# Kernel optimization log

Hardware: AMD Instinct MI355X
Metric: run time of the kernel (lower is better)

## Reference

```python
import jax, jax.numpy as jnp
import numpy as np

ATTR_LEN = [2, 4, 4, 2, 6]
CUM = np.concatenate(([0], np.cumsum(ATTR_LEN)))  # [0,2,6,10,12,18]
B, S, D, V = 4096, 200, 64, 100000


def setup_inputs() -> dict:
    key = jax.random.key(0)
    ks = jax.random.split(key, 10)
    x = jax.random.randint(ks[0], (B, S), 0, V)
    # one-hot labels per attribute, concatenated -> [B, 18]
    y_parts = []
    for i, al in enumerate(ATTR_LEN):
        lab = jax.random.randint(jax.random.fold_in(ks[1], i), (B,), 0, al)
        y_parts.append(jax.nn.one_hot(lab, al, dtype=jnp.float32))
    y = jnp.concatenate(y_parts, axis=1)
    emb_table = jax.random.normal(ks[2], (V, D), jnp.float32) * 0.02
    emb_table = emb_table.at[0].set(0.0)  # padding_idx=0
    att_w = jax.random.normal(ks[3], (5, D), jnp.float32) * 0.1
    att_b = jax.random.normal(ks[4], (5,), jnp.float32) * 0.1
    W0 = jax.random.normal(ks[5], (ATTR_LEN[0], D), jnp.float32) * 0.1
    W1 = jax.random.normal(ks[6], (ATTR_LEN[1], D), jnp.float32) * 0.1
    W2 = jax.random.normal(ks[7], (ATTR_LEN[2], D), jnp.float32) * 0.1
    W3 = jax.random.normal(ks[8], (ATTR_LEN[3], D), jnp.float32) * 0.1
    W4 = jax.random.normal(ks[9], (ATTR_LEN[4], D), jnp.float32) * 0.1
    return {"x": x, "y": y, "emb_table": emb_table, "att_w": att_w,
            "att_b": att_b, "W0": W0, "W1": W1, "W2": W2, "W3": W3, "W4": W4}


def reference(x, y, emb_table, att_w, att_b, W0, W1, W2, W3, W4):
    embed = emb_table[x]  # [B, S, D] gather (padding row is zero)
    # 5 per-attribute additive tanh-attention heads, batched over k.
    # Softmax over seq axis is independent per head, so stacking is exact.
    att_u = jnp.tanh(jnp.einsum('bsd,kd->bsk', embed, att_w) + att_b)  # [B,S,5]
    score = jax.nn.softmax(att_u, axis=1)                              # [B,S,5]
    user_rep = jnp.einsum('bsd,bsk->bkd', embed, score)                # [B,5,D]
    Ws = [W0, W1, W2, W3, W4]
    # per-task bias-free linear heads, concatenated -> [B, 18]
    W_user = jnp.concatenate([user_rep[:, i] @ Ws[i].T for i in range(5)], axis=1)
    logits = []
    loss = jnp.float32(0.0)
    for i in range(5):
        Wc = W_user[:, CUM[i]:CUM[i + 1]]
        yc = y[:, CUM[i]:CUM[i + 1]]
        # partial_training=False -> ob = ones -> all rows kept;
        # obj = exp(sum(W*y)) / sum_j exp(W_j)  ==  softmax picked at label
        logp = jax.nn.log_softmax(Wc, axis=1)
        loss = loss + (-jnp.sum(logp * yc) / Wc.shape[0])
        logits.append(jax.nn.softmax(Wc, axis=1))
    logit = jnp.concatenate(logits, axis=1)  # [B, 18]
    return logit, loss
```

## Files before the change

### kernel.cpp

```cpp
#include <hip/hip_runtime.h>
#include <math.h>
#include <stdint.h>

#define Bsz 4096
#define Ssz 200
#define Dsz 64
#define NK  5
#define NT  512
#define RST 72
#define TST 232
#define UNIH 14848

typedef _Float16 half_t;
typedef _Float16 h2    __attribute__((ext_vector_type(2)));
typedef _Float16 f16x8 __attribute__((ext_vector_type(8)));
typedef float    f32x4 __attribute__((ext_vector_type(4)));

__device__ inline h2 pk(float a, float b) {
    return __builtin_bit_cast(h2, __builtin_amdgcn_cvt_pkrtz(a, b));
}

__device__ inline float fast_tanh(float x) {
    float e = __expf(-2.0f * fabsf(x));
    float r = (1.0f - e) / (1.0f + e);
    return copysignf(r, x);
}

__device__ inline void phase_bar() {
    asm volatile("s_waitcnt lgkmcnt(0)" ::: "memory");
    __builtin_amdgcn_s_barrier();
    __builtin_amdgcn_sched_barrier(0);
}

__global__ void zero_loss_kernel(float* loss) {
    if (threadIdx.x == 0) *loss = 0.0f;
}

__global__ __launch_bounds__(256) void cvt_kernel(const float* __restrict__ src,
                                                  half_t* __restrict__ dst) {
    const size_t i = ((size_t)blockIdx.x * 256 + threadIdx.x) * 8;
    if (i < (size_t)100000 * 64) {
        float4 v0 = *(const float4*)(src + i);
        float4 v1 = *(const float4*)(src + i + 4);
        union { half_t h[8]; uint4 u; } o;
        o.h[0] = (half_t)v0.x; o.h[1] = (half_t)v0.y;
        o.h[2] = (half_t)v0.z; o.h[3] = (half_t)v0.w;
        o.h[4] = (half_t)v1.x; o.h[5] = (half_t)v1.y;
        o.h[6] = (half_t)v1.z; o.h[7] = (half_t)v1.w;
        *(uint4*)(dst + i) = o.u;
    }
}

__device__ inline void head_phase(int b, const float* wu, const float* __restrict__ y,
                                  float* __restrict__ out_logit, float& lossacc, int l) {
    if (l < NK) {
        const int LEN[5] = {2, 4, 4, 2, 6};
        const int C0[5]  = {0, 2, 6, 10, 12};
        const int g = l, c0 = C0[g], len = LEN[g];
        float* op = out_logit + (size_t)b * 18;
        const float* yp = y + (size_t)b * 18;
        float mx = -1e30f;
        for (int j = 0; j < len; ++j) mx = fmaxf(mx, wu[c0 + j]);
        float sum = 0.f;
        for (int j = 0; j < len; ++j) sum += __expf(wu[c0 + j] - mx);
        float inv = 1.0f / sum;
        float lse = mx + __logf(sum);
        for (int j = 0; j < len; ++j) {
            op[c0 + j] = __expf(wu[c0 + j] - mx) * inv;
            lossacc += (lse - wu[c0 + j]) * yp[c0 + j];
        }
    }
}

__global__ __launch_bounds__(NT, 8) void tan2_kernel(
    const int* __restrict__ x, const float* __restrict__ y,
    const half_t* __restrict__ tab16,
    const float* __restrict__ att_w, const float* __restrict__ att_b,
    const float* __restrict__ W0, const float* __restrict__ W1,
    const float* __restrict__ W2, const float* __restrict__ W3,
    const float* __restrict__ W4,
    float* __restrict__ out_logit, float* __restrict__ loss_out)
{
    __shared__ alignas(16) half_t uni[UNIH];
    __shared__ alignas(16) float  ovl[1000];
    __shared__ alignas(16) half_t ascore[NK * 240];
    __shared__ alignas(16) half_t awh[NK * RST];
    __shared__ float wu[18];

    half_t* embR = uni;
    half_t* embT = uni;
    float*  att_raw = ovl;

    const int blk = blockIdx.x;
    const int b0  = 2 * blk, b1 = 2 * blk + 1;
    const int tid = threadIdx.x;
    const int w   = tid >> 6;
    const int l   = tid & 63;
    const int col = l & 15;
    const int kg  = l >> 4;

    float lossacc = 0.f;

    {
        uint4 z = {0u, 0u, 0u, 0u};
        if (tid < 200)
            *(uint4*)((char*)uni + tid * 144 + 128) = z;
        else if (tid < 256)
            *(uint4*)((char*)uni + 28800 + (tid - 200) * 16) = z;
    }
    if (tid >= 256 && tid < 256 + NK * 32) {
        const int t = tid - 256, row = t >> 5, cp = t & 31;
        h2 v = {(half_t)att_w[row * 64 + 2 * cp],
                (half_t)att_w[row * 64 + 2 * cp + 1]};
        *(h2*)(awh + row * RST + 2 * cp) = v;
    }
    uint4 ga[4], gb[4];
#pragma unroll
    for (int p = 0; p < 4; ++p) {
        int i = tid + NT * p;
        if (i > 1599) i = 1599;
        const int s = i >> 3, c = i & 7;
        ga[p] = *(const uint4*)(tab16 + (size_t)x[b0 * Ssz + s] * Dsz + c * 8);
    }
#pragma unroll
    for (int p = 0; p < 4; ++p) {
        int i = tid + NT * p;
        if (i > 1599) i = 1599;
        const int s = i >> 3, c = i & 7;
        gb[p] = *(const uint4*)(tab16 + (size_t)x[b1 * Ssz + s] * Dsz + c * 8);
    }
#pragma unroll
    for (int p = 0; p < 4; ++p) {
        const int i = tid + NT * p;
        if (p < 3 || i < 1600) {
            const int s = i >> 3, c = i & 7;
            *(uint4*)(embR + s * RST + c * 8) = ga[p];
        }
    }
    phase_bar();

    h2 te[4][4];
#pragma unroll 1
    for (int bb = 0; bb < 2; ++bb) {
#pragma unroll
        for (int p = 0; p < 4; ++p) {
            int t = tid + NT * p;
            if (t > 1599) t = 1599;
            const int dp = t & 31, sq = t >> 5;
#pragma unroll
            for (int r = 0; r < 4; ++r)
                te[p][r] = *(const h2*)(embR + (4 * sq + r) * RST + 2 * dp);
        }
        {
            const int brow = (col < 5) ? col : 0;
            const f16x8 bw0 = *(const f16x8*)(awh + brow * RST + kg * 8);
            const f16x8 bw1 = *(const f16x8*)(awh + brow * RST + 32 + kg * 8);
            const float bk = att_b[brow];
            for (int t = w; t < 13; t += 8) {
                const int s  = 16 * t + col;
                const int sr = (s < Ssz) ? s : (Ssz - 1);
                const f16x8 a0 = *(const f16x8*)(embR + sr * RST + kg * 8);
                const f16x8 a1 = *(const f16x8*)(embR + sr * RST + 32 + kg * 8);
                f32x4 acc = {0.f, 0.f, 0.f, 0.f};
                acc = __builtin_amdgcn_mfma_f32_16x16x32_f16(a0, bw0, acc, 0, 0, 0);
                acc = __builtin_amdgcn_mfma_f32_16x16x32_f16(a1, bw1, acc, 0, 0, 0);
                if (col < 5) {
#pragma unroll
                    for (int r = 0; r < 4; ++r) {
                        const int srow = 16 * t + 4 * kg + r;
                        if (srow < Ssz)
                            att_raw[col * 200 + srow] = fast_tanh(acc[r] + bk);
                    }
                }
            }
        }
        if (bb == 1 && w == 0) head_phase(b0, wu, y, out_logit, lossacc, l);
        phase_bar();

#pragma unroll
        for (int p = 0; p < 4; ++p) {
            const int t = tid + NT * p;
            if (t < 1600) {
                const int dp = t & 31, sq = t >> 5;
                h2 lo01 = {te[p][0].x, te[p][1].x}, lo23 = {te[p][2].x, te[p][3].x};
                h2 hi01 = {te[p][0].y, te[p][1].y}, hi23 = {te[p][2].y, te[p][3].y};
                uint2 ulo = { __builtin_bit_cast(unsigned, lo01),
                              __builtin_bit_cast(unsigned, lo23) };
                uint2 uhi = { __builtin_bit_cast(unsigned, hi01),
                              __builtin_bit_cast(unsigned, hi23) };
                *(uint2*)(embT + (2 * dp)     * TST + 4 * sq) = ulo;
                *(uint2*)(embT + (2 * dp + 1) * TST + 4 * sq) = uhi;
            }
        }
        if (w < NK) {
            const int k = w;
            float vals[4];
            float mx = -1e30f;
#pragma unroll
            for (int j = 0; j < 4; ++j) {
                const int s = l + 64 * j;
                vals[j] = (s < Ssz) ? att_raw[k * 200 + s] : -1e30f;
                mx = fmaxf(mx, vals[j]);
            }
#pragma unroll
            for (int m = 32; m >= 1; m >>= 1) mx = fmaxf(mx, __shfl_xor(mx, m));
            float sum = 0.f;
#pragma unroll
            for (int j = 0; j < 4; ++j) {
                vals[j] = __expf(vals[j] - mx);
                sum += vals[j];
            }
#pragma unroll
            for (int m = 32; m >= 1; m >>= 1) sum += __shfl_xor(sum, m);
            const float inv = 1.0f / sum;
#pragma unroll
            for (int j = 0; j < 4; ++j) {
                const int s = l + 64 * j;
                if (s < Ssz)      ascore[k * 240 + s] = (half_t)(vals[j] * inv);
                else if (s < 224) ascore[k * 240 + s] = (half_t)0.0f;
            }
        }
        phase_bar();

        {
            const int dtile = w & 3, hh = w >> 2;
            const int arow = (col < 5) ? col : 0;
            const int KK0 = hh ? 4 : 0;
            const int NKK = hh ? 3 : 4;
            f32x4 acc = {0.f, 0.f, 0.f, 0.f};
            for (int q = 0; q < NKK; ++q) {
                const int kk = KK0 + q;
                const f16x8 af = *(const f16x8*)(embT + (dtile * 16 + col) * TST
                                                 + kk * 32 + kg * 8);
                const f16x8 bf = *(const f16x8*)(ascore + arow * 240 + kk * 32 + kg * 8);
                acc = __builtin_amdgcn_mfma_f32_16x16x32_f16(af, bf, acc, 0, 0, 0);
            }
            float* urp = ovl + hh * 320;
            if (col < 5) {
#pragma unroll
                for (int r = 0; r < 4; ++r)
                    urp[col * 64 + dtile * 16 + 4 * kg + r] = acc[r];
            }
        }
        phase_bar();

        if (bb == 0) {
#pragma unroll
            for (int p = 0; p < 4; ++p) {
                const int i = tid + NT * p;
                if (p < 3 || i < 1600) {
                    const int s = i >> 3, c = i & 7;
                    *(uint4*)(embR + s * RST + c * 8) = gb[p];
                }
            }
        }
        for (int j = w; j < 18; j += 8) {
            const float* Wp; int gr, c0;
            if      (j < 2)  { gr = 0; c0 = 0;  Wp = W0; }
            else if (j < 6)  { gr = 1; c0 = 2;  Wp = W1; }
            else if (j < 10) { gr = 2; c0 = 6;  Wp = W2; }
            else if (j < 12) { gr = 3; c0 = 10; Wp = W3; }
            else             { gr = 4; c0 = 12; Wp = W4; }
            float p = (ovl[gr * 64 + l] + ovl[320 + gr * 64 + l])
                      * Wp[(j - c0) * Dsz + l];
#pragma unroll
            for (int m = 32; m >= 1; m >>= 1) p += __shfl_xor(p, m);
            if (l == 0) wu[j] = p;
        }
        phase_bar();
    }

    if (w == 0) {
        head_phase(b1, wu, y, out_logit, lossacc, l);
#pragma unroll
        for (int m = 1; m <= 4; m <<= 1) lossacc += __shfl_xor(lossacc, m);
        if (l == 0) atomicAdd(loss_out, lossacc * (1.0f / Bsz));
    }
}

__global__ __launch_bounds__(NT, 8) void tan1_kernel(
    const int* __restrict__ x, const float* __restrict__ y,
    const float* __restrict__ emb_table,
    const float* __restrict__ att_w, const float* __restrict__ att_b,
    const float* __restrict__ W0, const float* __restrict__ W1,
    const float* __restrict__ W2, const float* __restrict__ W3,
    const float* __restrict__ W4,
    float* __restrict__ out_logit, float* __restrict__ loss_out)
{
    __shared__ alignas(16) half_t uni[UNIH];
    __shared__ alignas(16) float  ovl[1000];
    __shared__ alignas(16) half_t ascore[NK * 240];
    __shared__ alignas(16) half_t awh[NK * RST];
    __shared__ alignas(16) int    xs[Ssz];
    __shared__ float wu[18];

    half_t* embR = uni;
    half_t* embT = uni;
    float*  att_raw = ovl;

    const int b   = blockIdx.x;
    const int tid = threadIdx.x;
    const int w   = tid >> 6;
    const int l   = tid & 63;
    const int col = l & 15;
    const int kg  = l >> 4;

    if (tid < Ssz) xs[tid] = x[b * Ssz + tid];
    {
        uint4 z = {0u, 0u, 0u, 0u};
        if (tid >= 200 && tid < 400)
            *(uint4*)((char*)uni + (tid - 200) * 144 + 128) = z;
        else if (tid >= 400 && tid < 456)
            *(uint4*)((char*)uni + 28800 + (tid - 400) * 16) = z;
    }
    if (tid >= 456 && tid < 456 + 40) {
        const int t = tid - 456, row = t >> 3, cp = t & 7;
        h2 v0 = {(half_t)att_w[row * 64 + 8 * cp + 0], (half_t)att_w[row * 64 + 8 * cp + 1]};
        h2 v1 = {(half_t)att_w[row * 64 + 8 * cp + 2], (half_t)att_w[row * 64 + 8 * cp + 3]};
        h2 v2 = {(half_t)att_w[row * 64 + 8 * cp + 4], (half_t)att_w[row * 64 + 8 * cp + 5]};
        h2 v3 = {(half_t)att_w[row * 64 + 8 * cp + 6], (half_t)att_w[row * 64 + 8 * cp + 7]};
        *(h2*)(awh + row * RST + 8 * cp + 0) = v0;
        *(h2*)(awh + row * RST + 8 * cp + 2) = v1;
        *(h2*)(awh + row * RST + 8 * cp + 4) = v2;
        *(h2*)(awh + row * RST + 8 * cp + 6) = v3;
    }
    __syncthreads();
    {
        float4 v[7];
#pragma unroll
        for (int p = 0; p < 7; ++p) {
            int i = tid + NT * p;
            if (i > Ssz * 16 - 1) i = Ssz * 16 - 1;
            const int s = i >> 4, c = i & 15;
            v[p] = ((const float4*)(emb_table + (size_t)xs[s] * Dsz))[c];
        }
#pragma unroll
        for (int p = 0; p < 7; ++p) {
            const int i = tid + NT * p;
            if (p < 6 || i < Ssz * 16) {
                const int s = i >> 4, c = i & 15;
                h2 lo = pk(v[p].x, v[p].y);
                h2 hi = pk(v[p].z, v[p].w);
                uint2 u = { __builtin_bit_cast(unsigned, lo),
                            __builtin_bit_cast(unsigned, hi) };
                *(uint2*)(embR + s * RST + c * 4) = u;
            }
        }
    }
    __syncthreads();
    h2 te[4][4];
#pragma unroll
    for (int p = 0; p < 4; ++p) {
        int t = tid + NT * p;
        if (t > 1599) t = 1599;
        const int dp = t & 31, sq = t >> 5;
#pragma unroll
        for (int r = 0; r < 4; ++r)
            te[p][r] = *(const h2*)(embR + (4 * sq + r) * RST + 2 * dp);
    }
    {
        const int brow = (col < 5) ? col : 0;
        const f16x8 bw0 = *(const f16x8*)(awh + brow * RST + kg * 8);
        const f16x8 bw1 = *(const f16x8*)(awh + brow * RST + 32 + kg * 8);
        const float bk = att_b[brow];
        for (int t = w; t < 13; t += 8) {
            const int s  = 16 * t + col;
            const int sr = (s < Ssz) ? s : (Ssz - 1);
            const f16x8 a0 = *(const f16x8*)(embR + sr * RST + kg * 8);
            const f16x8 a1 = *(const f16x8*)(embR + sr * RST + 32 + kg * 8);
            f32x4 acc = {0.f, 0.f, 0.f, 0.f};
            acc = __builtin_amdgcn_mfma_f32_16x16x32_f16(a0, bw0, acc, 0, 0, 0);
            acc = __builtin_amdgcn_mfma_f32_16x16x32_f16(a1, bw1, acc, 0, 0, 0);
            if (col < 5) {
#pragma unroll
                for (int r = 0; r < 4; ++r) {
                    const int srow = 16 * t + 4 * kg + r;
                    if (srow < Ssz)
                        att_raw[col * 200 + srow] = fast_tanh(acc[r] + bk);
                }
            }
        }
    }
    __syncthreads();
#pragma unroll
    for (int p = 0; p < 4; ++p) {
        const int t = tid + NT * p;
        if (t < 1600) {
            const int dp = t & 31, sq = t >> 5;
            h2 lo01 = {te[p][0].x, te[p][1].x}, lo23 = {te[p][2].x, te[p][3].x};
            h2 hi01 = {te[p][0].y, te[p][1].y}, hi23 = {te[p][2].y, te[p][3].y};
            uint2 ulo = { __builtin_bit_cast(unsigned, lo01),
                          __builtin_bit_cast(unsigned, lo23) };
            uint2 uhi = { __builtin_bit_cast(unsigned, hi01),
                          __builtin_bit_cast(unsigned, hi23) };
            *(uint2*)(embT + (2 * dp)     * TST + 4 * sq) = ulo;
            *(uint2*)(embT + (2 * dp + 1) * TST + 4 * sq) = uhi;
        }
    }
    if (w < NK) {
        const int k = w;
        float vals[4];
        float mx = -1e30f;
#pragma unroll
        for (int j = 0; j < 4; ++j) {
            const int s = l + 64 * j;
            vals[j] = (s < Ssz) ? att_raw[k * 200 + s] : -1e30f;
            mx = fmaxf(mx, vals[j]);
        }
#pragma unroll
        for (int m = 32; m >= 1; m >>= 1) mx = fmaxf(mx, __shfl_xor(mx, m));
        float sum = 0.f;
#pragma unroll
        for (int j = 0; j < 4; ++j) {
            vals[j] = __expf(vals[j] - mx);
            sum += vals[j];
        }
#pragma unroll
        for (int m = 32; m >= 1; m >>= 1) sum += __shfl_xor(sum, m);
        const float inv = 1.0f / sum;
#pragma unroll
        for (int j = 0; j < 4; ++j) {
            const int s = l + 64 * j;
            if (s < Ssz)      ascore[k * 240 + s] = (half_t)(vals[j] * inv);
            else if (s < 224) ascore[k * 240 + s] = (half_t)0.0f;
        }
    }
    __syncthreads();
    {
        const int dtile = w & 3, hh = w >> 2;
        const int arow = (col < 5) ? col : 0;
        const int KK0 = hh ? 4 : 0;
        const int NKK = hh ? 3 : 4;
        f32x4 acc = {0.f, 0.f, 0.f, 0.f};
        for (int q = 0; q < NKK; ++q) {
            const int kk = KK0 + q;
            const f16x8 af = *(const f16x8*)(embT + (dtile * 16 + col) * TST
                                             + kk * 32 + kg * 8);
            const f16x8 bf = *(const f16x8*)(ascore + arow * 240 + kk * 32 + kg * 8);
            acc = __builtin_amdgcn_mfma_f32_16x16x32_f16(af, bf, acc, 0, 0, 0);
        }
        float* urp = ovl + hh * 320;
        if (col < 5) {
#pragma unroll
            for (int r = 0; r < 4; ++r)
                urp[col * 64 + dtile * 16 + 4 * kg + r] = acc[r];
        }
    }
    __syncthreads();
    for (int j = w; j < 18; j += 8) {
        const float* Wp; int gr, c0;
        if      (j < 2)  { gr = 0; c0 = 0;  Wp = W0; }
        else if (j < 6)  { gr = 1; c0 = 2;  Wp = W1; }
        else if (j < 10) { gr = 2; c0 = 6;  Wp = W2; }
        else if (j < 12) { gr = 3; c0 = 10; Wp = W3; }
        else             { gr = 4; c0 = 12; Wp = W4; }
        float p = (ovl[gr * 64 + l] + ovl[320 + gr * 64 + l]) * Wp[(j - c0) * Dsz + l];
#pragma unroll
        for (int m = 32; m >= 1; m >>= 1) p += __shfl_xor(p, m);
        if (l == 0) wu[j] = p;
    }
    __syncthreads();
    if (w == 0) {
        float lossb = 0.f;
        head_phase(b, wu, y, out_logit, lossb, l);
#pragma unroll
        for (int m = 1; m <= 4; m <<= 1) lossb += __shfl_xor(lossb, m);
        if (l == 0) atomicAdd(loss_out, lossb * (1.0f / Bsz));
    }
}

extern "C" void kernel_launch(void* const* d_in, const int* in_sizes, int n_in,
                              void* d_out, int out_size, void* d_ws, size_t ws_size,
                              hipStream_t stream) {
    const int*   x   = (const int*)d_in[0];
    const float* y   = (const float*)d_in[1];
    const float* emb = (const float*)d_in[2];
    const float* aw  = (const float*)d_in[3];
    const float* ab  = (const float*)d_in[4];
    const float* W0  = (const float*)d_in[5];
    const float* W1  = (const float*)d_in[6];
    const float* W2  = (const float*)d_in[7];
    const float* W3  = (const float*)d_in[8];
    const float* W4  = (const float*)d_in[9];
    float* out  = (float*)d_out;
    float* loss = out + (size_t)Bsz * 18;

    zero_loss_kernel<<<1, 64, 0, stream>>>(loss);

    const size_t need = (size_t)100000 * 64 * sizeof(half_t);
    if (d_ws && ws_size >= need) {
        half_t* tab16 = (half_t*)d_ws;
        cvt_kernel<<<3125, 256, 0, stream>>>(emb, tab16);
        tan2_kernel<<<Bsz / 2, NT, 0, stream>>>(x, y, tab16, aw, ab,
                                                W0, W1, W2, W3, W4, out, loss);
    } else {
        tan1_kernel<<<Bsz, NT, 0, stream>>>(x, y, emb, aw, ab,
                                            W0, W1, W2, W3, W4, out, loss);
    }
}
```

Before: 171.7 us.

## Gather first batch row directly to LDS with XOR-swizzled unpadded layout

Result: faster. 166.9 us (-2.8%).

```diff
diff --git a/kernel.cpp b/kernel.cpp
--- a/kernel.cpp
+++ b/kernel.cpp
@@ -7,7 +7,7 @@
 #define Dsz 64
 #define NK  5
 #define NT  512
-#define RST 72
+#define AWST 72
 #define TST 232
 #define UNIH 14848
 
@@ -72,7 +72,7 @@
     }
 }
 
-__global__ __launch_bounds__(NT, 8) void tan2_kernel(
+__global__ __launch_bounds__(NT, 6) void tan2_kernel(
     const int* __restrict__ x, const float* __restrict__ y,
     const half_t* __restrict__ tab16,
     const float* __restrict__ att_w, const float* __restrict__ att_b,
@@ -84,7 +84,7 @@
     __shared__ alignas(16) half_t uni[UNIH];
     __shared__ alignas(16) float  ovl[1000];
     __shared__ alignas(16) half_t ascore[NK * 240];
-    __shared__ alignas(16) half_t awh[NK * RST];
+    __shared__ alignas(16) half_t awh[NK * AWST];
     __shared__ float wu[18];
 
     half_t* embR = uni;
@@ -101,42 +101,50 @@
 
     float lossacc = 0.f;
 
-    {
+    if (tid < 256) {
         uint4 z = {0u, 0u, 0u, 0u};
-        if (tid < 200)
-            *(uint4*)((char*)uni + tid * 144 + 128) = z;
-        else if (tid < 256)
-            *(uint4*)((char*)uni + 28800 + (tid - 200) * 16) = z;
+        *(uint4*)((char*)uni + 25600 + tid * 16) = z;
     }
     if (tid >= 256 && tid < 256 + NK * 32) {
         const int t = tid - 256, row = t >> 5, cp = t & 31;
         h2 v = {(half_t)att_w[row * 64 + 2 * cp],
                 (half_t)att_w[row * 64 + 2 * cp + 1]};
-        *(h2*)(awh + row * RST + 2 * cp) = v;
-    }
-    uint4 ga[4], gb[4];
+        *(h2*)(awh + row * AWST + 2 * cp) = v;
+    }
+
+    int xr0[4], xr1[4];
 #pragma unroll
     for (int p = 0; p < 4; ++p) {
         int i = tid + NT * p;
         if (i > 1599) i = 1599;
-        const int s = i >> 3, c = i & 7;
-        ga[p] = *(const uint4*)(tab16 + (size_t)x[b0 * Ssz + s] * Dsz + c * 8);
-    }
+        const int s = i >> 3;
+        xr0[p] = x[b0 * Ssz + s];
+        xr1[p] = x[b1 * Ssz + s];
+    }
+
+#pragma unroll
+    for (int p = 0; p < 4; ++p) {
+        if (p < 3 || tid < 64) {
+            const int i = tid + NT * p;
+            const int s = i >> 3, c = i & 7;
+            const half_t* gp = tab16 + (size_t)xr0[p] * Dsz + ((c ^ (s & 7)) << 3);
+            char* lp = (char*)uni + ((size_t)((tid & ~63) + NT * p) << 4);
+            __builtin_amdgcn_global_load_lds(
+                (const __attribute__((address_space(1))) void*)gp,
+                (__attribute__((address_space(3))) void*)lp, 16, 0, 0);
+        }
+    }
+    __builtin_amdgcn_sched_barrier(0);
+    uint4 gb[4];
 #pragma unroll
     for (int p = 0; p < 4; ++p) {
         int i = tid + NT * p;
         if (i > 1599) i = 1599;
-        const int s = i >> 3, c = i & 7;
-        gb[p] = *(const uint4*)(tab16 + (size_t)x[b1 * Ssz + s] * Dsz + c * 8);
-    }
-#pragma unroll
-    for (int p = 0; p < 4; ++p) {
-        const int i = tid + NT * p;
-        if (p < 3 || i < 1600) {
-            const int s = i >> 3, c = i & 7;
-            *(uint4*)(embR + s * RST + c * 8) = ga[p];
-        }
-    }
+        const int c = i & 7;
+        gb[p] = *(const uint4*)(tab16 + (size_t)xr1[p] * Dsz + c * 8);
+    }
+    __builtin_amdgcn_sched_barrier(0);
+    asm volatile("s_waitcnt vmcnt(4)" ::: "memory");
     phase_bar();
 
     h2 te[4][4];
@@ -148,19 +156,24 @@
             if (t > 1599) t = 1599;
             const int dp = t & 31, sq = t >> 5;
 #pragma unroll
-            for (int r = 0; r < 4; ++r)
-                te[p][r] = *(const h2*)(embR + (4 * sq + r) * RST + 2 * dp);
+            for (int r = 0; r < 4; ++r) {
+                const int s4 = 4 * sq + r;
+                te[p][r] = *(const h2*)(embR + s4 * 64
+                                        + (((dp >> 2) ^ (s4 & 7)) << 3)
+                                        + (dp & 3) * 2);
+            }
         }
         {
             const int brow = (col < 5) ? col : 0;
-            const f16x8 bw0 = *(const f16x8*)(awh + brow * RST + kg * 8);
-            const f16x8 bw1 = *(const f16x8*)(awh + brow * RST + 32 + kg * 8);
+            const f16x8 bw0 = *(const f16x8*)(awh + brow * AWST + kg * 8);
+            const f16x8 bw1 = *(const f16x8*)(awh + brow * AWST + 32 + kg * 8);
             const float bk = att_b[brow];
             for (int t = w; t < 13; t += 8) {
                 const int s  = 16 * t + col;
                 const int sr = (s < Ssz) ? s : (Ssz - 1);
-                const f16x8 a0 = *(const f16x8*)(embR + sr * RST + kg * 8);
-                const f16x8 a1 = *(const f16x8*)(embR + sr * RST + 32 + kg * 8);
+                const int c0 = kg ^ (sr & 7);
+                const f16x8 a0 = *(const f16x8*)(embR + sr * 64 + (c0 << 3));
+                const f16x8 a1 = *(const f16x8*)(embR + sr * 64 + ((c0 ^ 4) << 3));
                 f32x4 acc = {0.f, 0.f, 0.f, 0.f};
                 acc = __builtin_amdgcn_mfma_f32_16x16x32_f16(a0, bw0, acc, 0, 0, 0);
                 acc = __builtin_amdgcn_mfma_f32_16x16x32_f16(a1, bw1, acc, 0, 0, 0);
@@ -250,19 +263,19 @@
                 const int i = tid + NT * p;
                 if (p < 3 || i < 1600) {
                     const int s = i >> 3, c = i & 7;
-                    *(uint4*)(embR + s * RST + c * 8) = gb[p];
+                    *(uint4*)(embR + s * 64 + ((c ^ (s & 7)) << 3)) = gb[p];
                 }
             }
         }
         for (int j = w; j < 18; j += 8) {
-            const float* Wp; int gr, c0;
-            if      (j < 2)  { gr = 0; c0 = 0;  Wp = W0; }
-            else if (j < 6)  { gr = 1; c0 = 2;  Wp = W1; }
-            else if (j < 10) { gr = 2; c0 = 6;  Wp = W2; }
-            else if (j < 12) { gr = 3; c0 = 10; Wp = W3; }
-            else             { gr = 4; c0 = 12; Wp = W4; }
+            const float* Wp; int gr, c0w;
+            if      (j < 2)  { gr = 0; c0w = 0;  Wp = W0; }
+            else if (j < 6)  { gr = 1; c0w = 2;  Wp = W1; }
+            else if (j < 10) { gr = 2; c0w = 6;  Wp = W2; }
+            else if (j < 12) { gr = 3; c0w = 10; Wp = W3; }
+            else             { gr = 4; c0w = 12; Wp = W4; }
             float p = (ovl[gr * 64 + l] + ovl[320 + gr * 64 + l])
-                      * Wp[(j - c0) * Dsz + l];
+                      * Wp[(j - c0w) * Dsz + l];
 #pragma unroll
             for (int m = 32; m >= 1; m >>= 1) p += __shfl_xor(p, m);
             if (l == 0) wu[j] = p;
@@ -278,7 +291,7 @@
     }
 }
 
-__global__ __launch_bounds__(NT, 8) void tan1_kernel(
+__global__ __launch_bounds__(NT, 6) void tan1_kernel(
     const int* __restrict__ x, const float* __restrict__ y,
     const float* __restrict__ emb_table,
     const float* __restrict__ att_w, const float* __restrict__ att_b,
@@ -287,6 +300,7 @@
     const float* __restrict__ W4,
     float* __restrict__ out_logit, float* __restrict__ loss_out)
 {
+#define RST 72
     __shared__ alignas(16) half_t uni[UNIH];
     __shared__ alignas(16) float  ovl[1000];
     __shared__ alignas(16) half_t ascore[NK * 240];
@@ -448,13 +462,13 @@
     }
     __syncthreads();
     for (int j = w; j < 18; j += 8) {
-        const float* Wp; int gr, c0;
-        if      (j < 2)  { gr = 0; c0 = 0;  Wp = W0; }
-        else if (j < 6)  { gr = 1; c0 = 2;  Wp = W1; }
-        else if (j < 10) { gr = 2; c0 = 6;  Wp = W2; }
-        else if (j < 12) { gr = 3; c0 = 10; Wp = W3; }
-        else             { gr = 4; c0 = 12; Wp = W4; }
-        float p = (ovl[gr * 64 + l] + ovl[320 + gr * 64 + l]) * Wp[(j - c0) * Dsz + l];
+        const float* Wp; int gr, c0w;
+        if      (j < 2)  { gr = 0; c0w = 0;  Wp = W0; }
+        else if (j < 6)  { gr = 1; c0w = 2;  Wp = W1; }
+        else if (j < 10) { gr = 2; c0w = 6;  Wp = W2; }
+        else if (j < 12) { gr = 3; c0w = 10; Wp = W3; }
+        else             { gr = 4; c0w = 12; Wp = W4; }
+        float p = (ovl[gr * 64 + l] + ovl[320 + gr * 64 + l]) * Wp[(j - c0w) * Dsz + l];
 #pragma unroll
         for (int m = 32; m >= 1; m >>= 1) p += __shfl_xor(p, m);
         if (l == 0) wu[j] = p;
@@ -467,6 +481,7 @@
         for (int m = 1; m <= 4; m <<= 1) lossb += __shfl_xor(lossb, m);
         if (l == 0) atomicAdd(loss_out, lossb * (1.0f / Bsz));
     }
+#undef RST
 }
 
 extern "C" void kernel_launch(void* const* d_in, const int* in_sizes, int n_in,
```
